# Kernel tuning notes

Measured on AMD Instinct MI355X. Metric: run time of the kernel, lower is better.

The kernel has to match this reference:

```python
import jax, jax.numpy as jnp
import numpy as np

B, S, E = 2, 2048, 2048
A, H = 2048, 16  # attention_dim, n_heads
HD = A // H      # head_dim = 128
ROPE_THETA = 10000.0


def setup_inputs() -> dict:
    key = jax.random.key(0)
    k1, k2, k3 = jax.random.split(key, 3)
    x = jax.random.normal(k1, (B, S, E), dtype=jnp.float32)
    W_qkv = jax.random.normal(k2, (E, 3 * A), dtype=jnp.float32) * 0.02
    W_out = jax.random.normal(k3, (A, E), dtype=jnp.float32) * 0.02
    return {"x": x, "W_qkv": W_qkv, "W_out": W_out}


def _apply_rope(x):
    # x: (B, H, S, D); interleaved rotary pairs (rotary-embedding-torch default)
    b, h, s, d = x.shape
    inv_freq = 1.0 / (ROPE_THETA ** (jnp.arange(0, d, 2, dtype=jnp.float32) / d))
    freqs = jnp.arange(s, dtype=jnp.float32)[:, None] * inv_freq[None, :]  # (S, D/2)
    cos, sin = jnp.cos(freqs), jnp.sin(freqs)
    xr = x.reshape(b, h, s, d // 2, 2)
    x1, x2 = xr[..., 0], xr[..., 1]
    o1 = x1 * cos - x2 * sin
    o2 = x1 * sin + x2 * cos
    return jnp.stack([o1, o2], axis=-1).reshape(b, h, s, d)


def reference(x, W_qkv, W_out):
    b, s, _ = x.shape
    qkv = (x @ W_qkv).reshape(b, s, 3, H, HD)          # (B,S,3,H,hd)
    qkv = jnp.moveaxis(qkv, 3, 1)                      # movedim(-2,1) -> (B,H,S,3,hd)
    q, k, v = qkv[..., 0, :], qkv[..., 1, :], qkv[..., 2, :]
    q = _apply_rope(q)
    k = _apply_rope(k)
    scale = 1.0 / jnp.sqrt(jnp.asarray(HD, dtype=x.dtype))
    scores = jnp.einsum("bhqd,bhkd->bhqk", q, k) * scale
    attn = jax.nn.softmax(scores, axis=-1)
    out = jnp.einsum("bhqk,bhkd->bhqd", attn, v)       # (B,H,S,hd)
    out = out.transpose(0, 2, 1, 3).reshape(b, s, A)   # (B,S,A)
    return out @ W_out
```

## Files before the change

### kernel.cpp

```cpp
#include <hip/hip_runtime.h>
#include <math.h>

typedef float  f32x4  __attribute__((ext_vector_type(4)));
typedef short  s16x8 __attribute__((ext_vector_type(8)));
typedef short  s16x4 __attribute__((ext_vector_type(4)));
typedef unsigned short u16;
typedef unsigned int u32;

static __device__ __forceinline__ u16 f32_to_bf16_rne(float f) {
    u32 u = __builtin_bit_cast(u32, f);
    u32 r = u + 0x7fffu + ((u >> 16) & 1u);
    return (u16)(r >> 16);
}
static __device__ __forceinline__ u32 pack_bf16_rhu(float a, float b) {
    u32 ua = __builtin_bit_cast(u32, a);
    u32 ub = __builtin_bit_cast(u32, b);
    return ((ua + 0x8000u) >> 16) | ((ub + 0x8000u) & 0xffff0000u);
}

static __device__ __forceinline__ void gl2lds16(const void* g, void* l) {
    __builtin_amdgcn_global_load_lds(
        (const __attribute__((address_space(1))) u32*)g,
        (__attribute__((address_space(3))) u32*)l, 16, 0, 0);
}


__global__ __launch_bounds__(256) void k_prep(const float* __restrict__ x,
                                              const float* __restrict__ Wq,
                                              const float* __restrict__ Wo,
                                              u16* __restrict__ xb,
                                              u16* __restrict__ Wqt,
                                              u16* __restrict__ Wot) {
    __shared__ float TT[64 * 130];
    const int blk = blockIdx.x;
    const int t = threadIdx.x;
    if (blk < 4096) {
        int i = (blk * 256 + t) * 8;
        float4 a = *reinterpret_cast<const float4*>(x + i);
        float4 b = *reinterpret_cast<const float4*>(x + i + 4);
        s16x8 o;
        o[0] = (short)f32_to_bf16_rne(a.x); o[1] = (short)f32_to_bf16_rne(a.y);
        o[2] = (short)f32_to_bf16_rne(a.z); o[3] = (short)f32_to_bf16_rne(a.w);
        o[4] = (short)f32_to_bf16_rne(b.x); o[5] = (short)f32_to_bf16_rne(b.y);
        o[6] = (short)f32_to_bf16_rne(b.z); o[7] = (short)f32_to_bf16_rne(b.w);
        *reinterpret_cast<s16x8*>(xb + i) = o;
        return;
    }
    const float* in; u16* out; int C, ct, rt; bool perm;
    if (blk < 5632) {
        int tb = blk - 4096; ct = tb % 96; rt = tb / 96; in = Wq; out = Wqt; C = 6144; perm = true;
    } else {
        int tb = blk - 5632; ct = tb % 32; rt = tb / 32; in = Wo; out = Wot; C = 2048; perm = false;
    }
    const int R = 2048;
    const int tr = t >> 4, tc = t & 15;
    float4 v[8];
#pragma unroll
    for (int u = 0; u < 8; ++u) {
        int r = u * 16 + tr;
        v[u] = *reinterpret_cast<const float4*>(in + (size_t)(rt * 128 + r) * C + ct * 64 + tc * 4);
    }
#pragma unroll
    for (int u = 0; u < 8; ++u) {
        int r = u * 16 + tr;
        TT[(tc * 4 + 0) * 130 + r] = v[u].x;
        TT[(tc * 4 + 1) * 130 + r] = v[u].y;
        TT[(tc * 4 + 2) * 130 + r] = v[u].z;
        TT[(tc * 4 + 3) * 130 + r] = v[u].w;
    }
    __syncthreads();
#pragma unroll
    for (int u = 0; u < 4; ++u) {
        int oc = u * 16 + tr;
        int r0 = tc * 8;
        s16x8 o;
#pragma unroll
        for (int e = 0; e < 8; ++e)
            o[e] = (short)f32_to_bf16_rne(TT[oc * 130 + r0 + e]);
        int n = ct * 64 + oc;
        int nn = n;
        if (perm) {
            if (n < 4096) nn = (n >> 8) * 384 + (n & 255);
            else { int vv = n - 4096; nn = (vv >> 7) * 384 + 256 + (vv & 127); }
        }
        *reinterpret_cast<s16x8*>(out + (size_t)nn * R + rt * 128 + r0) = o;
    }
}

__global__ __launch_bounds__(512, 2) void k_gemm384(const u16* __restrict__ Amat,
                                                    const u16* __restrict__ Bt,
                                                    u16* __restrict__ Cout,
                                                    u16* __restrict__ Vt,
                                                    int M, int N, int K) {
    __shared__ __align__(16) u16 SMEM[2 * 128 * 64 + 2 * 384 * 64];
    const int AS_SZ = 128 * 64, BS_SZ = 384 * 64;
    const int t = threadIdx.x;
    const int lane = t & 63, wave = t >> 6;
    const int m16 = lane & 15, qd = lane >> 4;
    const int wr = wave >> 2, wc = wave & 3;
    const int srow = lane >> 3;
    const int sch = (lane & 7) ^ srow;

    int bx, by;
    if (gridDim.x == 16 && gridDim.y == 32) {
        int orig = blockIdx.y * gridDim.x + blockIdx.x;
        int xcd = orig & 7, loc = orig >> 3;
        int cx = xcd & 3, cy = xcd >> 2;
        bx = cx * 4 + (loc & 3);
        by = cy * 16 + (loc >> 2);
    } else {
        bx = blockIdx.x; by = blockIdx.y;
    }
    const size_t m0 = (size_t)by * 128, n0 = (size_t)bx * 384;

    const u16* Ab = Amat + m0 * (size_t)K;
    const u16* Bb = Bt + n0 * (size_t)K;
    const int NT = K >> 6;

    auto stage128 = [&](const u16* gbase, u16* lbase, int k0) {
        int rb0 = wave * 8;
        gl2lds16(gbase + (size_t)(rb0 + srow) * K + k0 + sch * 8, lbase + rb0 * 64);
        int rb1 = rb0 + 64;
        gl2lds16(gbase + (size_t)(rb1 + srow) * K + k0 + sch * 8, lbase + rb1 * 64);
    };

    f32x4 acc[4][6] = {};
    s16x8 af[4][2], bq[6][2];

    {
        u16* A0 = SMEM;
        u16* B0 = SMEM + 2 * AS_SZ;
        stage128(Bb,                   B0,            0);
        stage128(Bb + 128 * (size_t)K, B0 + 128 * 64, 0);
        stage128(Bb + 256 * (size_t)K, B0 + 256 * 64, 0);
        stage128(Ab,                   A0,            0);
        if (NT > 1) {
            u16* B1 = B0 + BS_SZ;
            stage128(Bb,                   B1,            64);
            stage128(Bb + 128 * (size_t)K, B1 + 128 * 64, 64);
            asm volatile("s_waitcnt vmcnt(4)" ::: "memory");
        } else {
            asm volatile("s_waitcnt vmcnt(0)" ::: "memory");
        }
    }
    __builtin_amdgcn_s_barrier();

    for (int kt = 0; kt < NT; ++kt) {
        const int p = kt & 1;
        u16* Ap  = SMEM + p * AS_SZ;
        u16* Bp  = SMEM + 2 * AS_SZ + p * BS_SZ;
        u16* Anx = SMEM + (p ^ 1) * AS_SZ;
        u16* Bnx = SMEM + 2 * AS_SZ + (p ^ 1) * BS_SZ;

#pragma unroll
        for (int i = 0; i < 4; ++i) {
            int ra = wr * 64 + i * 16 + m16;
            af[i][0] = *reinterpret_cast<const s16x8*>(&Ap[ra * 64 + ((qd)     ^ (ra & 7)) * 8]);
        }
#pragma unroll
        for (int j = 0; j < 6; ++j) {
            int rb = wc * 96 + j * 16 + m16;
            bq[j][0] = *reinterpret_cast<const s16x8*>(&Bp[rb * 64 + ((qd)     ^ (rb & 7)) * 8]);
        }
        if (kt + 1 < NT) stage128(Bb + 256 * (size_t)K, Bnx + 256 * 64, (kt + 1) << 6);
#pragma unroll
        for (int i = 0; i < 4; ++i) {
            int ra = wr * 64 + i * 16 + m16;
            af[i][1] = *reinterpret_cast<const s16x8*>(&Ap[ra * 64 + ((4 + qd) ^ (ra & 7)) * 8]);
        }
#pragma unroll
        for (int j = 0; j < 6; ++j) {
            int rb = wc * 96 + j * 16 + m16;
            bq[j][1] = *reinterpret_cast<const s16x8*>(&Bp[rb * 64 + ((4 + qd) ^ (rb & 7)) * 8]);
        }
        if (kt + 1 < NT) stage128(Ab, Anx, (kt + 1) << 6);

        __builtin_amdgcn_s_setprio(1);
#pragma unroll
        for (int i = 0; i < 4; ++i)
#pragma unroll
            for (int j = 0; j < 6; ++j)
                acc[i][j] = __builtin_amdgcn_mfma_f32_16x16x32_bf16(af[i][0], bq[j][0], acc[i][j], 0, 0, 0);
        __builtin_amdgcn_s_setprio(0);

        asm volatile("s_waitcnt lgkmcnt(0)" ::: "memory");
        __builtin_amdgcn_s_barrier();

        if (kt + 2 < NT) {
            stage128(Bb,                   Bp,            (kt + 2) << 6);
            stage128(Bb + 128 * (size_t)K, Bp + 128 * 64, (kt + 2) << 6);
        }
        __builtin_amdgcn_s_setprio(1);
#pragma unroll
        for (int i = 0; i < 4; ++i)
#pragma unroll
            for (int j = 0; j < 6; ++j)
                acc[i][j] = __builtin_amdgcn_mfma_f32_16x16x32_bf16(af[i][1], bq[j][1], acc[i][j], 0, 0, 0);
        __builtin_amdgcn_s_setprio(0);
        if (kt + 2 < NT) {
            asm volatile("s_waitcnt vmcnt(4)" ::: "memory");
        } else {
            asm volatile("s_waitcnt vmcnt(0)" ::: "memory");
        }
        __builtin_amdgcn_s_barrier();
    }

    {
        u16* VS = SMEM;
        float invf[6];
#pragma unroll
        for (int j = 0; j < 6; ++j) {
            int lc = wc * 96 + j * 16;
            if (lc < 256) {
                int oc = bx * 256 + lc + m16;
                invf[j] = __expf(-0.14391156831f * (float)((oc & 127) >> 1));
            } else invf[j] = 0.f;
        }
#pragma unroll
        for (int i = 0; i < 4; ++i)
#pragma unroll
            for (int j = 0; j < 6; ++j) {
                int lc = wc * 96 + j * 16;
                if (lc < 256) {
                    int oc = bx * 256 + lc + m16;
#pragma unroll
                    for (int r = 0; r < 4; ++r) {
                        float v = acc[i][j][r];
                        float pv = __shfl_xor(v, 1);
                        size_t row = m0 + wr * 64 + i * 16 + qd * 4 + r;
                        float f = (float)(int)(row & 2047) * invf[j];
                        float sn, cs;
                        __sincosf(f, &sn, &cs);
                        float res = (m16 & 1) ? fmaf(pv, sn, v * cs) : fmaf(v, cs, -pv * sn);
                        Cout[row * N + oc] = f32_to_bf16_rne(res);
                    }
                } else {
                    int d = lc - 256 + m16;
                    int sl = wr * 64 + i * 16 + qd * 4;
                    s16x4 o;
#pragma unroll
                    for (int r = 0; r < 4; ++r)
                        o[r] = (short)f32_to_bf16_rne(acc[i][j][r]);
                    *reinterpret_cast<s16x4*>(&VS[d * 130 + sl]) = o;
                }
            }
        __syncthreads();
        int b = (int)(m0 >> 11);
        int sbase = (int)(m0 & 2047);
        u16* vdst = Vt + ((size_t)(b * 16 + bx)) * 262144;
        int d = t >> 2, sc = t & 3;
#pragma unroll
        for (int e = 0; e < 4; ++e) {
            int s = sc * 8 + e * 32;
            s16x8 o = *reinterpret_cast<const s16x8*>(&VS[d * 130 + s]);
            *reinterpret_cast<s16x8*>(vdst + (size_t)d * 2048 + sbase + s) = o;
        }
    }
}

__global__ __launch_bounds__(512, 2) void k_gemmo(const u16* __restrict__ Amat,
                                                  const u16* __restrict__ Bt,
                                                  float* __restrict__ Cout,
                                                  int M, int N, int K) {
    __shared__ __align__(16) u16 As[2][128 * 64];
    __shared__ __align__(16) u16 Bs[2][256 * 64];
    const int t = threadIdx.x;
    const int lane = t & 63, wave = t >> 6;
    const int m16 = lane & 15, qd = lane >> 4;
    const int wr = wave >> 2, wc = wave & 3;
    const int srow = lane >> 3;
    const int sch = (lane & 7) ^ srow;

    int bx, by;
    if (gridDim.x == 8 && gridDim.y == 32) {
        int orig = blockIdx.y * gridDim.x + blockIdx.x;
        int xcd = orig & 7, loc = orig >> 3;
        int cx = xcd & 1, cy = xcd >> 1;
        bx = cx * 4 + (loc & 3);
        by = cy * 8 + (loc >> 2);
    } else {
        bx = blockIdx.x; by = blockIdx.y;
    }
    const size_t m0 = (size_t)by * 128, n0 = (size_t)bx * 256;

    const u16* Ab = Amat + m0 * (size_t)K;
    const u16* Bb = Bt + n0 * (size_t)K;
    const int NT = K >> 6;

    auto stage128 = [&](const u16* gbase, u16* lbase, int k0) {
        int rb0 = wave * 8;
        gl2lds16(gbase + (size_t)(rb0 + srow) * K + k0 + sch * 8, lbase + rb0 * 64);
        int rb1 = rb0 + 64;
        gl2lds16(gbase + (size_t)(rb1 + srow) * K + k0 + sch * 8, lbase + rb1 * 64);
    };

    f32x4 acc[4][4] = {};
    s16x8 af[4][2], bq[4][2];

    stage128(Ab,                   &As[0][0],        0);
    stage128(Bb,                   &Bs[0][0],        0);
    stage128(Bb + 128 * (size_t)K, &Bs[0][128 * 64], 0);
    if (NT > 1) {
        stage128(Ab,               &As[1][0],        64);
        stage128(Bb,               &Bs[1][0],        64);
        asm volatile("s_waitcnt vmcnt(4)" ::: "memory");
    } else {
        asm volatile("s_waitcnt vmcnt(0)" ::: "memory");
    }
    __builtin_amdgcn_s_barrier();

    for (int kt = 0; kt < NT; ++kt) {
        const int p = kt & 1;

#pragma unroll
        for (int i = 0; i < 4; ++i) {
            int ra = wr * 64 + i * 16 + m16;
            af[i][0] = *reinterpret_cast<const s16x8*>(&As[p][ra * 64 + ((qd)     ^ (ra & 7)) * 8]);
        }
#pragma unroll
        for (int j = 0; j < 4; ++j) {
            int rb = wc * 64 + j * 16 + m16;
            bq[j][0] = *reinterpret_cast<const s16x8*>(&Bs[p][rb * 64 + ((qd)     ^ (rb & 7)) * 8]);
        }
        if (kt + 1 < NT) stage128(Bb + 128 * (size_t)K, &Bs[p ^ 1][128 * 64], (kt + 1) << 6);
#pragma unroll
        for (int i = 0; i < 4; ++i) {
            int ra = wr * 64 + i * 16 + m16;
            af[i][1] = *reinterpret_cast<const s16x8*>(&As[p][ra * 64 + ((4 + qd) ^ (ra & 7)) * 8]);
        }
#pragma unroll
        for (int j = 0; j < 4; ++j) {
            int rb = wc * 64 + j * 16 + m16;
            bq[j][1] = *reinterpret_cast<const s16x8*>(&Bs[p][rb * 64 + ((4 + qd) ^ (rb & 7)) * 8]);
        }

        __builtin_amdgcn_s_setprio(1);
#pragma unroll
        for (int i = 0; i < 4; ++i)
#pragma unroll
            for (int j = 0; j < 4; ++j)
                acc[i][j] = __builtin_amdgcn_mfma_f32_16x16x32_bf16(af[i][0], bq[j][0], acc[i][j], 0, 0, 0);
        __builtin_amdgcn_s_setprio(0);

        asm volatile("s_waitcnt lgkmcnt(0)" ::: "memory");
        __builtin_amdgcn_s_barrier();

        if (kt + 2 < NT) {
            stage128(Ab, &As[p][0], (kt + 2) << 6);
            stage128(Bb, &Bs[p][0], (kt + 2) << 6);
        }
        __builtin_amdgcn_s_setprio(1);
#pragma unroll
        for (int i = 0; i < 4; ++i)
#pragma unroll
            for (int j = 0; j < 4; ++j)
                acc[i][j] = __builtin_amdgcn_mfma_f32_16x16x32_bf16(af[i][1], bq[j][1], acc[i][j], 0, 0, 0);
        __builtin_amdgcn_s_setprio(0);
        if (kt + 2 < NT) {
            asm volatile("s_waitcnt vmcnt(4)" ::: "memory");
        } else {
            asm volatile("s_waitcnt vmcnt(0)" ::: "memory");
        }
        __builtin_amdgcn_s_barrier();
    }

#pragma unroll
    for (int i = 0; i < 4; ++i)
#pragma unroll
        for (int j = 0; j < 4; ++j)
#pragma unroll
            for (int r = 0; r < 4; ++r) {
                size_t row = m0 + wr * 64 + i * 16 + qd * 4 + r;
                size_t col = n0 + wc * 64 + j * 16 + m16;
                Cout[row * N + col] = acc[i][j][r];
            }
}

__global__ __launch_bounds__(512, 4) void k_flash(const u16* __restrict__ qkv,
                                                  const u16* __restrict__ vt,
                                                  u16* __restrict__ out) {
    __shared__ __align__(16) u16 KS[128 * 136];
    __shared__ __align__(16) u16 VS[128 * 136];
    const int t = threadIdx.x, lane = t & 63, wave = t >> 6;
    const int m16 = lane & 15, qd = lane >> 4;
    const int bh = blockIdx.y, b = bh >> 4, h = bh & 15;
    const int q0 = blockIdx.x * 128;
    const u16* Qg = qkv + (size_t)b * 2048 * 6144 + (size_t)h * 128;
    const u16* Kg = Qg + 2048;
    const u16* Vtg = vt + (size_t)bh * 128 * 2048;
    const float C2 = 0.12751743f;

    int srow[4], scol[4], pi0[4];
#pragma unroll
    for (int ci = 0; ci < 4; ++ci) {
        int idx = ci * 512 + t;
        int row = idx >> 4, c = idx & 15;
        srow[ci] = row;
        scol[ci] = c * 8;
        pi0[ci] = 32 * (c >> 2) + 16 * (c & 1) + 4 * ((c >> 1) & 1);
    }

    s16x8 qf[4];
#pragma unroll
    for (int kc = 0; kc < 4; ++kc)
        qf[kc] = *reinterpret_cast<const s16x8*>(
            Qg + (size_t)(q0 + wave * 16 + m16) * 6144 + kc * 32 + qd * 8);

    f32x4 accO[8] = {};
    float mrow = -1e30f, lrow = 0.f;

    for (int kt = 0; kt < 16; ++kt) {
        const int s0 = kt * 128;
        s16x8 kreg[4], vreg[4];
#pragma unroll
        for (int ci = 0; ci < 4; ++ci) {
            kreg[ci] = *reinterpret_cast<const s16x8*>(
                Kg + (size_t)(s0 + srow[ci]) * 6144 + scol[ci]);
            vreg[ci] = *reinterpret_cast<const s16x8*>(
                Vtg + (size_t)srow[ci] * 2048 + s0 + scol[ci]);
        }
        __syncthreads();
#pragma unroll
        for (int ci = 0; ci < 4; ++ci) {
            *reinterpret_cast<s16x8*>(&KS[srow[ci] * 136 + scol[ci]]) = kreg[ci];
            s16x4 lo = __builtin_shufflevector(vreg[ci], vreg[ci], 0, 1, 2, 3);
            s16x4 hi = __builtin_shufflevector(vreg[ci], vreg[ci], 4, 5, 6, 7);
            *reinterpret_cast<s16x4*>(&VS[srow[ci] * 136 + pi0[ci]]) = lo;
            *reinterpret_cast<s16x4*>(&VS[srow[ci] * 136 + pi0[ci] + 8]) = hi;
        }
        __syncthreads();

        f32x4 accS[8] = {};
#pragma unroll
        for (int kc = 0; kc < 4; ++kc)
#pragma unroll
            for (int nj = 0; nj < 8; ++nj) {
                s16x8 kf = *reinterpret_cast<const s16x8*>(
                    &KS[(nj * 16 + m16) * 136 + (kc * 4 + qd) * 8]);
                accS[nj] = __builtin_amdgcn_mfma_f32_16x16x32_bf16(kf, qf[kc], accS[nj], 0, 0, 0);
            }

        float mx = accS[0][0];
#pragma unroll
        for (int nj = 0; nj < 8; ++nj)
#pragma unroll
            for (int r = 0; r < 4; ++r) mx = fmaxf(mx, accS[nj][r]);
        mx *= C2;
        mx = fmaxf(mx, __shfl_xor(mx, 16));
        mx = fmaxf(mx, __shfl_xor(mx, 32));
        float mn = fmaxf(mrow, mx);
        float alpha = __builtin_amdgcn_exp2f(mrow - mn);
        mrow = mn;
        float ls = 0.f;
        s16x4 pk[8];
#pragma unroll
        for (int nj = 0; nj < 8; ++nj) {
            float p0 = __builtin_amdgcn_exp2f(fmaf(accS[nj][0], C2, -mn));
            float p1 = __builtin_amdgcn_exp2f(fmaf(accS[nj][1], C2, -mn));
            float p2 = __builtin_amdgcn_exp2f(fmaf(accS[nj][2], C2, -mn));
            float p3 = __builtin_amdgcn_exp2f(fmaf(accS[nj][3], C2, -mn));
            ls += (p0 + p1) + (p2 + p3);
            u32 lo = pack_bf16_rhu(p0, p1);
            u32 hi = pack_bf16_rhu(p2, p3);
            uint2 pr = make_uint2(lo, hi);
            pk[nj] = __builtin_bit_cast(s16x4, pr);
        }
        ls += __shfl_xor(ls, 16);
        ls += __shfl_xor(ls, 32);
        lrow = lrow * alpha + ls;
        float aO[4];
#pragma unroll
        for (int r = 0; r < 4; ++r) aO[r] = __shfl(alpha, qd * 4 + r);
#pragma unroll
        for (int dj = 0; dj < 8; ++dj)
#pragma unroll
            for (int r = 0; r < 4; ++r) accO[dj][r] *= aO[r];

#pragma unroll
        for (int kb = 0; kb < 4; ++kb) {
            s16x8 af = __builtin_shufflevector(pk[2 * kb], pk[2 * kb + 1],
                                               0, 1, 2, 3, 4, 5, 6, 7);
#pragma unroll
            for (int dj = 0; dj < 8; ++dj) {
                s16x8 vf = *reinterpret_cast<const s16x8*>(
                    &VS[(dj * 16 + m16) * 136 + kb * 32 + qd * 8]);
                accO[dj] = __builtin_amdgcn_mfma_f32_16x16x32_bf16(af, vf, accO[dj], 0, 0, 0);
            }
        }
    }
    float invl = 1.0f / lrow;
    float iv[4];
#pragma unroll
    for (int r = 0; r < 4; ++r) iv[r] = __shfl(invl, qd * 4 + r);
#pragma unroll
    for (int r = 0; r < 4; ++r) {
        size_t row = (size_t)b * 2048 + q0 + wave * 16 + qd * 4 + r;
#pragma unroll
        for (int dj = 0; dj < 8; ++dj)
            out[row * 2048 + h * 128 + dj * 16 + m16] =
                f32_to_bf16_rne(accO[dj][r] * iv[r]);
    }
}

extern "C" void kernel_launch(void* const* d_in, const int* in_sizes, int n_in,
                              void* d_out, int out_size, void* d_ws, size_t ws_size,
                              hipStream_t stream) {
    const float* x     = (const float*)d_in[0];
    const float* W_qkv = (const float*)d_in[1];
    const float* W_out = (const float*)d_in[2];
    float* out = (float*)d_out;

    char* ws = (char*)d_ws;
    u16* xb   = (u16*)(ws);
    u16* Wqt  = (u16*)(ws + (16u << 20));
    u16* Wot  = (u16*)(ws + (40u << 20));
    u16* qkvb = (u16*)(ws + (48u << 20));
    u16* attn = (u16*)(ws + (96u << 20));
    u16* vtg  = (u16*)(ws + (112u << 20));

    k_prep<<<6144, 256, 0, stream>>>(x, W_qkv, W_out, xb, Wqt, Wot);
    k_gemm384<<<dim3(16, 32), 512, 0, stream>>>(xb, Wqt, qkvb, vtg, 4096, 6144, 2048);
    k_flash<<<dim3(16, 32), 512, 0, stream>>>(qkvb, vtg, attn);
    k_gemmo<<<dim3(8, 32), 512, 0, stream>>>(attn, Wot, out, 4096, 2048, 2048);
}
```

Baseline: 396.8 us.

## Double-buffer K/V tiles in flash attention with 64-key tiles and register prefetch

The flash-attention kernel now uses two LDS buffers for K and V with 64-key tiles instead of one buffer with 128-key tiles. Each iteration writes the next tile from registers into the spare buffer and issues global loads two tiles ahead while computing on the current one. This cuts the barriers per tile from two to one and hides global load latency behind the MFMA work. In exchange there are twice as many iterations, each with more softmax rescale overhead per key, and tighter register pressure from the prefetch registers.

```diff
diff --git a/kernel.cpp b/kernel.cpp
--- a/kernel.cpp
+++ b/kernel.cpp
@@ -379,8 +379,8 @@
 __global__ __launch_bounds__(512, 4) void k_flash(const u16* __restrict__ qkv,
                                                   const u16* __restrict__ vt,
                                                   u16* __restrict__ out) {
-    __shared__ __align__(16) u16 KS[128 * 136];
-    __shared__ __align__(16) u16 VS[128 * 136];
+    __shared__ __align__(16) u16 KS[2][64 * 136];
+    __shared__ __align__(16) u16 VS[2][128 * 72];
     const int t = threadIdx.x, lane = t & 63, wave = t >> 6;
     const int m16 = lane & 15, qd = lane >> 4;
     const int bh = blockIdx.y, b = bh >> 4, h = bh & 15;
@@ -390,14 +390,15 @@
     const u16* Vtg = vt + (size_t)bh * 128 * 2048;
     const float C2 = 0.12751743f;
 
-    int srow[4], scol[4], pi0[4];
-#pragma unroll
-    for (int ci = 0; ci < 4; ++ci) {
+    int krow[2], kcol[2], vrow[2], vsc[2], vpi[2];
+#pragma unroll
+    for (int ci = 0; ci < 2; ++ci) {
         int idx = ci * 512 + t;
-        int row = idx >> 4, c = idx & 15;
-        srow[ci] = row;
-        scol[ci] = c * 8;
-        pi0[ci] = 32 * (c >> 2) + 16 * (c & 1) + 4 * ((c >> 1) & 1);
+        krow[ci] = idx >> 4; kcol[ci] = (idx & 15) * 8;
+        vrow[ci] = idx >> 3;
+        int vc = idx & 7;
+        vsc[ci] = vc * 8;
+        vpi[ci] = 32 * (vc >> 2) + 16 * (vc & 1) + 4 * ((vc >> 1) & 1);
     }
 
     s16x8 qf[4];
@@ -409,40 +410,65 @@
     f32x4 accO[8] = {};
     float mrow = -1e30f, lrow = 0.f;
 
-    for (int kt = 0; kt < 16; ++kt) {
-        const int s0 = kt * 128;
-        s16x8 kreg[4], vreg[4];
-#pragma unroll
-        for (int ci = 0; ci < 4; ++ci) {
-            kreg[ci] = *reinterpret_cast<const s16x8*>(
-                Kg + (size_t)(s0 + srow[ci]) * 6144 + scol[ci]);
-            vreg[ci] = *reinterpret_cast<const s16x8*>(
-                Vtg + (size_t)srow[ci] * 2048 + s0 + scol[ci]);
-        }
-        __syncthreads();
-#pragma unroll
-        for (int ci = 0; ci < 4; ++ci) {
-            *reinterpret_cast<s16x8*>(&KS[srow[ci] * 136 + scol[ci]]) = kreg[ci];
-            s16x4 lo = __builtin_shufflevector(vreg[ci], vreg[ci], 0, 1, 2, 3);
-            s16x4 hi = __builtin_shufflevector(vreg[ci], vreg[ci], 4, 5, 6, 7);
-            *reinterpret_cast<s16x4*>(&VS[srow[ci] * 136 + pi0[ci]]) = lo;
-            *reinterpret_cast<s16x4*>(&VS[srow[ci] * 136 + pi0[ci] + 8]) = hi;
-        }
-        __syncthreads();
-
-        f32x4 accS[8] = {};
+    s16x8 kreg[2], vreg[2];
+#pragma unroll
+    for (int ci = 0; ci < 2; ++ci) {
+        kreg[ci] = *reinterpret_cast<const s16x8*>(Kg + (size_t)krow[ci] * 6144 + kcol[ci]);
+        vreg[ci] = *reinterpret_cast<const s16x8*>(Vtg + (size_t)vrow[ci] * 2048 + vsc[ci]);
+    }
+#pragma unroll
+    for (int ci = 0; ci < 2; ++ci) {
+        *reinterpret_cast<s16x8*>(&KS[0][krow[ci] * 136 + kcol[ci]]) = kreg[ci];
+        s16x4 lo = __builtin_shufflevector(vreg[ci], vreg[ci], 0, 1, 2, 3);
+        s16x4 hi = __builtin_shufflevector(vreg[ci], vreg[ci], 4, 5, 6, 7);
+        *reinterpret_cast<s16x4*>(&VS[0][vrow[ci] * 72 + vpi[ci]]) = lo;
+        *reinterpret_cast<s16x4*>(&VS[0][vrow[ci] * 72 + vpi[ci] + 8]) = hi;
+    }
+#pragma unroll
+    for (int ci = 0; ci < 2; ++ci) {
+        kreg[ci] = *reinterpret_cast<const s16x8*>(Kg + (size_t)(64 + krow[ci]) * 6144 + kcol[ci]);
+        vreg[ci] = *reinterpret_cast<const s16x8*>(Vtg + (size_t)vrow[ci] * 2048 + 64 + vsc[ci]);
+    }
+    asm volatile("s_waitcnt lgkmcnt(0)" ::: "memory");
+    __builtin_amdgcn_s_barrier();
+
+    for (int kt = 0; kt < 32; ++kt) {
+        const int bsel = kt & 1;
+
+        if (kt + 1 < 32) {
+#pragma unroll
+            for (int ci = 0; ci < 2; ++ci) {
+                *reinterpret_cast<s16x8*>(&KS[bsel ^ 1][krow[ci] * 136 + kcol[ci]]) = kreg[ci];
+                s16x4 lo = __builtin_shufflevector(vreg[ci], vreg[ci], 0, 1, 2, 3);
+                s16x4 hi = __builtin_shufflevector(vreg[ci], vreg[ci], 4, 5, 6, 7);
+                *reinterpret_cast<s16x4*>(&VS[bsel ^ 1][vrow[ci] * 72 + vpi[ci]]) = lo;
+                *reinterpret_cast<s16x4*>(&VS[bsel ^ 1][vrow[ci] * 72 + vpi[ci] + 8]) = hi;
+            }
+        }
+        if (kt + 2 < 32) {
+            const int sn = (kt + 2) * 64;
+#pragma unroll
+            for (int ci = 0; ci < 2; ++ci) {
+                kreg[ci] = *reinterpret_cast<const s16x8*>(
+                    Kg + (size_t)(sn + krow[ci]) * 6144 + kcol[ci]);
+                vreg[ci] = *reinterpret_cast<const s16x8*>(
+                    Vtg + (size_t)vrow[ci] * 2048 + sn + vsc[ci]);
+            }
+        }
+
+        f32x4 accS[4] = {};
 #pragma unroll
         for (int kc = 0; kc < 4; ++kc)
 #pragma unroll
-            for (int nj = 0; nj < 8; ++nj) {
+            for (int nj = 0; nj < 4; ++nj) {
                 s16x8 kf = *reinterpret_cast<const s16x8*>(
-                    &KS[(nj * 16 + m16) * 136 + (kc * 4 + qd) * 8]);
+                    &KS[bsel][(nj * 16 + m16) * 136 + (kc * 4 + qd) * 8]);
                 accS[nj] = __builtin_amdgcn_mfma_f32_16x16x32_bf16(kf, qf[kc], accS[nj], 0, 0, 0);
             }
 
         float mx = accS[0][0];
 #pragma unroll
-        for (int nj = 0; nj < 8; ++nj)
+        for (int nj = 0; nj < 4; ++nj)
 #pragma unroll
             for (int r = 0; r < 4; ++r) mx = fmaxf(mx, accS[nj][r]);
         mx *= C2;
@@ -452,9 +478,9 @@
         float alpha = __builtin_amdgcn_exp2f(mrow - mn);
         mrow = mn;
         float ls = 0.f;
-        s16x4 pk[8];
-#pragma unroll
-        for (int nj = 0; nj < 8; ++nj) {
+        s16x4 pk[4];
+#pragma unroll
+        for (int nj = 0; nj < 4; ++nj) {
             float p0 = __builtin_amdgcn_exp2f(fmaf(accS[nj][0], C2, -mn));
             float p1 = __builtin_amdgcn_exp2f(fmaf(accS[nj][1], C2, -mn));
             float p2 = __builtin_amdgcn_exp2f(fmaf(accS[nj][2], C2, -mn));
@@ -477,16 +503,19 @@
             for (int r = 0; r < 4; ++r) accO[dj][r] *= aO[r];
 
 #pragma unroll
-        for (int kb = 0; kb < 4; ++kb) {
+        for (int kb = 0; kb < 2; ++kb) {
             s16x8 af = __builtin_shufflevector(pk[2 * kb], pk[2 * kb + 1],
                                                0, 1, 2, 3, 4, 5, 6, 7);
 #pragma unroll
             for (int dj = 0; dj < 8; ++dj) {
                 s16x8 vf = *reinterpret_cast<const s16x8*>(
-                    &VS[(dj * 16 + m16) * 136 + kb * 32 + qd * 8]);
+                    &VS[bsel][(dj * 16 + m16) * 72 + kb * 32 + qd * 8]);
                 accO[dj] = __builtin_amdgcn_mfma_f32_16x16x32_bf16(af, vf, accO[dj], 0, 0, 0);
             }
         }
+
+        asm volatile("s_waitcnt lgkmcnt(0)" ::: "memory");
+        __builtin_amdgcn_s_barrier();
     }
     float invl = 1.0f / lrow;
     float iv[4];
```

Measured after the change: 382.9 us. 3.5% less time.
